# Kernel optimization log

Measured on AMD Instinct MI355X. Metric: run time of the kernel, lower is better.

The kernel has to match this reference:

```python
import jax, jax.numpy as jnp
import numpy as np

D_MODEL = 1024
B, N = 2, 4096
EPS = 1e-4


def setup_inputs() -> dict:
    key = jax.random.key(0)
    ks = jax.random.split(key, 8)
    s = 1.0 / np.sqrt(D_MODEL)
    return {
        "x": jax.random.normal(ks[0], (B, N, D_MODEL), dtype=jnp.float32),
        "Wq": jax.random.normal(ks[1], (D_MODEL, D_MODEL), dtype=jnp.float32) * s,
        "bq": jax.random.normal(ks[2], (D_MODEL,), dtype=jnp.float32) * 0.01,
        "Wk": jax.random.normal(ks[3], (D_MODEL, D_MODEL), dtype=jnp.float32) * s,
        "bk": jax.random.normal(ks[4], (D_MODEL,), dtype=jnp.float32) * 0.01,
        "Wv": jax.random.normal(ks[5], (D_MODEL, D_MODEL), dtype=jnp.float32) * s,
        "bv": jax.random.normal(ks[6], (D_MODEL,), dtype=jnp.float32) * 0.01,
        "alpha": jnp.float32(1.5),
        "lam": jnp.float32(12.0),
    }


def reference(x, Wq, bq, Wk, bk, Wv, bv, alpha, lam):
    # CSOCKernelAttention.forward
    Bb, n, d = x.shape
    # torch nn.Linear: y = x @ W.T + b
    q = jnp.einsum("bnd,ed->bne", x, Wq) + bq
    k = jnp.einsum("bnd,ed->bne", x, Wk) + bk
    v = jnp.einsum("bnd,ed->bne", x, Wv) + bv
    idx = jnp.arange(n, dtype=jnp.float32)
    r = jnp.abs(idx[:, None] - idx[None, :])  # [N, N]
    # K(r) = (r + eps)^(-|alpha|) * exp(-r / |lambda|)
    K = (r + EPS) ** (-jnp.abs(alpha)) * jnp.exp(-r / jnp.abs(lam))  # [N, N]
    logits = jnp.einsum("bqd,bkd->bqk", q, k) / jnp.sqrt(jnp.float32(d))
    logits = logits * K[None]
    attn = jax.nn.softmax(logits, axis=-1)
    out = jnp.einsum("bqk,bkd->bqd", attn, v)
    return (out, attn, K)
```

## Files before the change

### kernel.cpp

```cpp
#include <hip/hip_runtime.h>
#include <hip/hip_bf16.h>
#include <cstdint>
#include <cstddef>

#define D_MODEL 1024
#define SEQ_N   4096
#define BATCH   2
#define BAND    256
#define NELEM   ((size_t)BATCH * SEQ_N * D_MODEL)

typedef __attribute__((ext_vector_type(4))) float  floatx4;
typedef __attribute__((ext_vector_type(8))) short  short8;
typedef __attribute__((ext_vector_type(4))) short  short4v;

__device__ __forceinline__ unsigned short f2bf(float f) {
  unsigned u = __float_as_uint(f);
  u += 0x7FFFu + ((u >> 16) & 1u);
  return (unsigned short)(u >> 16);
}
__device__ __forceinline__ float bf2f(unsigned short u) {
  return __uint_as_float(((unsigned)u) << 16);
}

__global__ __launch_bounds__(256)
void fused_prep(const float* __restrict__ x,
                const float* __restrict__ Wq, const float* __restrict__ Wk,
                const float* __restrict__ Wv, const float* __restrict__ bv,
                const float* __restrict__ alpha_p, const float* __restrict__ lam_p,
                unsigned short* __restrict__ xb,
                unsigned short* __restrict__ Bcat2,
                unsigned short* __restrict__ wqT,
                unsigned short* __restrict__ wkT,
                float* __restrict__ bias2,
                float* __restrict__ K1d)
{
  __shared__ unsigned short Tld[64][66];
  int bid = blockIdx.x, tid = threadIdx.x;
  if (bid < 4096) {
    int i = bid * 256 + tid;
    const floatx4* s4 = (const floatx4*)x;
    floatx4 a = s4[i * 2], b = s4[i * 2 + 1];
    short8 pk;
    pk[0] = (short)f2bf(a[0]); pk[1] = (short)f2bf(a[1]);
    pk[2] = (short)f2bf(a[2]); pk[3] = (short)f2bf(a[3]);
    pk[4] = (short)f2bf(b[0]); pk[5] = (short)f2bf(b[1]);
    pk[6] = (short)f2bf(b[2]); pk[7] = (short)f2bf(b[3]);
    *(short8*)(xb + (size_t)i * 8) = pk;
  } else if (bid < 4608) {
    int i = (bid - 4096) * 256 + tid;
    const floatx4* s4 = (const floatx4*)Wv;
    floatx4 a = s4[i * 2], b = s4[i * 2 + 1];
    short8 pk;
    pk[0] = (short)f2bf(a[0]); pk[1] = (short)f2bf(a[1]);
    pk[2] = (short)f2bf(a[2]); pk[3] = (short)f2bf(a[3]);
    pk[4] = (short)f2bf(b[0]); pk[5] = (short)f2bf(b[1]);
    pk[6] = (short)f2bf(b[2]); pk[7] = (short)f2bf(b[3]);
    *(short8*)(Bcat2 + (size_t)D_MODEL * D_MODEL + (size_t)i * 8) = pk;
  } else if (bid < 5120) {
    int u = bid - 4608;
    const float* src = (u < 256) ? Wq : Wk;
    unsigned short* dst = (u < 256) ? wqT : wkT;
    int t = u & 255;
    int tr = t >> 4, tc = t & 15;
    int rl = tid >> 2, cc = (tid & 3) * 16;
    const float* sp = src + (size_t)(tr * 64 + rl) * D_MODEL + tc * 64 + cc;
#pragma unroll
    for (int q4 = 0; q4 < 4; ++q4) {
      floatx4 v = *(const floatx4*)(sp + q4 * 4);
#pragma unroll
      for (int e = 0; e < 4; ++e) Tld[cc + q4 * 4 + e][rl] = f2bf(v[e]);
    }
    __syncthreads();
    int cl = tid >> 2, rchunk = (tid & 3) * 16;
    short8 o0, o1;
#pragma unroll
    for (int e = 0; e < 8; ++e) { o0[e] = (short)Tld[cl][rchunk + e]; o1[e] = (short)Tld[cl][rchunk + 8 + e]; }
    unsigned short* dp = dst + (size_t)(tc * 64 + cl) * D_MODEL + tr * 64 + rchunk;
    *(short8*)dp = o0;
    *(short8*)(dp + 8) = o1;
  } else {
    int t = (bid - 5120) * 256 + tid;
    if (t < SEQ_N) {
      float a   = fabsf(alpha_p[0]);
      float lam = fabsf(lam_p[0]);
      float rf  = (float)t;
      K1d[t] = powf(rf + 1e-4f, -a) * expf(-rf / lam);
    }
    int v = t - SEQ_N;
    if (v >= 0 && v < D_MODEL) bias2[D_MODEL + v] = bv[v];
  }
}

__global__ __launch_bounds__(256)
void wtilde_kernel(const unsigned short* __restrict__ wkT,
                   const unsigned short* __restrict__ wqT,
                   const float* __restrict__ bq, const float* __restrict__ bk,
                   float* __restrict__ bias2, float* __restrict__ wqv)
{
  const int lane = threadIdx.x & 63, wave = threadIdx.x >> 6;
  const int idx = blockIdx.x * 4 + wave;
  const int d = idx & (D_MODEL - 1);
  const bool isK = idx < D_MODEL;
  const unsigned short* row = (isK ? wkT : wqT) + (size_t)d * D_MODEL + lane * 16;
  const float* b = isK ? bq : bk;
  float s = 0.f;
  short8 v0 = *(const short8*)row, v1 = *(const short8*)(row + 8);
#pragma unroll
  for (int e = 0; e < 8; ++e) {
    s += bf2f((unsigned short)v0[e]) * b[lane * 16 + e];
    s += bf2f((unsigned short)v1[e]) * b[lane * 16 + 8 + e];
  }
#pragma unroll
  for (int o = 32; o; o >>= 1) s += __shfl_xor(s, o);
  if (lane == 0) { if (isK) bias2[d] = s; else wqv[d] = s; }
}

__global__ __launch_bounds__(256)
void rho_kernel(const unsigned short* __restrict__ xb, const float* __restrict__ wqv,
                const float* __restrict__ bq, const float* __restrict__ bk,
                float* __restrict__ rho)
{
  const int lane = threadIdx.x & 63, wave = threadIdx.x >> 6;
  const int gi = blockIdx.x * 4 + wave;
  const unsigned short* xr = xb + (size_t)gi * D_MODEL + lane * 16;
  float s1 = 0.f, s2 = 0.f;
  short8 v0 = *(const short8*)xr, v1 = *(const short8*)(xr + 8);
#pragma unroll
  for (int e = 0; e < 8; ++e) {
    s1 += bf2f((unsigned short)v0[e]) * wqv[lane * 16 + e];
    s1 += bf2f((unsigned short)v1[e]) * wqv[lane * 16 + 8 + e];
  }
#pragma unroll
  for (int e = 0; e < 16; ++e)
    s2 += bq[lane * 16 + e] * bk[lane * 16 + e];
  float s = s1 + s2;
#pragma unroll
  for (int o = 32; o; o >>= 1) s += __shfl_xor(s, o);
  if (lane == 0) rho[gi] = s;
}

__global__ void k1d_kernel(float* __restrict__ K1d,
                           const float* __restrict__ alpha_p,
                           const float* __restrict__ lam_p) {
  int r = blockIdx.x * blockDim.x + threadIdx.x;
  if (r >= SEQ_N) return;
  float a   = fabsf(alpha_p[0]);
  float lam = fabsf(lam_p[0]);
  float rf  = (float)r;
  K1d[r] = powf(rf + 1e-4f, -a) * expf(-rf / lam);
}

__global__ __launch_bounds__(256) void writeK_kernel(float* __restrict__ Kout,
                                                     const float* __restrict__ K1d) {
  size_t t = (size_t)blockIdx.x * 256 + threadIdx.x;
  size_t f = t * 4;
  int i = (int)(f >> 12);
  int j = (int)(f & 4095);
  floatx4 v;
#pragma unroll
  for (int e = 0; e < 4; ++e) {
    int d = i - (j + e); d = d < 0 ? -d : d;
    v[e] = K1d[d];
  }
  __builtin_nontemporal_store(v, (floatx4*)(Kout + f));
}

__global__ __launch_bounds__(256)
void gemm64_mt(const unsigned short* __restrict__ A,
               const unsigned short* __restrict__ B,
               unsigned short* __restrict__ C)
{
  __shared__ unsigned short As[64 * 32];
  __shared__ unsigned short Bs[64 * 32];
  const int tid = threadIdx.x, lane = tid & 63, wave = tid >> 6;
  int gx = (int)gridDim.x;
  int total = gx * (int)gridDim.y;
  int flat  = (int)blockIdx.y * gx + (int)blockIdx.x;
  int w     = (flat & 7) * (total >> 3) + (flat >> 3);
  int bx = w % gx, by = w / gx;
  const int bm0 = by * 64, bn0 = bx * 64;
  const int wm = (wave >> 1) * 32, wn = (wave & 1) * 32;

  floatx4 acc[2][2] = {};
  for (int k0 = 0; k0 < D_MODEL; k0 += 32) {
    {
      int bu = wave * 64;
      int u  = bu + lane;
      const unsigned short* srcA = A + (size_t)(bm0 + (u >> 2)) * D_MODEL + k0 + (u & 3) * 8;
      __builtin_amdgcn_global_load_lds((const __attribute__((address_space(1))) void*)srcA,
                                       (__attribute__((address_space(3))) void*)(As + bu * 8), 16, 0, 0);
      const unsigned short* srcB = B + (size_t)(bn0 + (u >> 2)) * D_MODEL + k0 + (u & 3) * 8;
      __builtin_amdgcn_global_load_lds((const __attribute__((address_space(1))) void*)srcB,
                                       (__attribute__((address_space(3))) void*)(Bs + bu * 8), 16, 0, 0);
    }
    __syncthreads();
    short8 af[2], bf[2];
#pragma unroll
    for (int i = 0; i < 2; ++i)
      af[i] = *(const short8*)(As + (wm + i * 16 + (lane & 15)) * 32 + (lane >> 4) * 8);
#pragma unroll
    for (int j = 0; j < 2; ++j)
      bf[j] = *(const short8*)(Bs + (wn + j * 16 + (lane & 15)) * 32 + (lane >> 4) * 8);
#pragma unroll
    for (int i = 0; i < 2; ++i)
#pragma unroll
      for (int j = 0; j < 2; ++j)
        acc[i][j] = __builtin_amdgcn_mfma_f32_16x16x32_bf16(af[i], bf[j], acc[i][j], 0, 0, 0);
    __syncthreads();
  }
#pragma unroll
  for (int i = 0; i < 2; ++i) {
#pragma unroll
    for (int j = 0; j < 2; ++j) {
      int col   = bn0 + wn + j * 16 + (lane & 15);
      int rbase = bm0 + wm + i * 16 + (lane >> 4) * 4;
#pragma unroll
      for (int r = 0; r < 4; ++r)
        C[(size_t)(rbase + r) * D_MODEL + col] = f2bf(acc[i][j][r]);
    }
  }
}

__global__ __launch_bounds__(256)
void uv_gemm(const unsigned short* __restrict__ xb,
             const unsigned short* __restrict__ Bcat2,
             const float* __restrict__ bias2,
             unsigned short* __restrict__ ub,
             unsigned short* __restrict__ vT)
{
  __shared__ unsigned short As[128 * 64];
  __shared__ unsigned short Bs[128 * 64];
  const int tid = threadIdx.x, lane = tid & 63, wave = tid >> 6;

  int gx = (int)gridDim.x, gy = (int)gridDim.y;
  int total = gx * gy;
  int flat  = (int)blockIdx.y * gx + (int)blockIdx.x;
  int w     = (flat & 7) * (total >> 3) + (flat >> 3);
  int bx = w % gx, by = w / gx;
  const int bm0 = by * 128;
  const int bn0 = bx * 128;
  const int wm = (wave >> 1) * 64, wn = (wave & 1) * 64;
  const bool isU = (bn0 < D_MODEL);

  floatx4 acc[4][4] = {};
  for (int k0 = 0; k0 < D_MODEL; k0 += 64) {
#pragma unroll
    for (int t = 0; t < 4; ++t) {
      int bu  = wave * 64 + t * 256;
      int u   = bu + lane;
      int row = u >> 3;
      int c   = (u & 7) ^ (row & 7);
      const unsigned short* srcA = xb + (size_t)(bm0 + row) * D_MODEL + k0 + c * 8;
      __builtin_amdgcn_global_load_lds((const __attribute__((address_space(1))) void*)srcA,
                                       (__attribute__((address_space(3))) void*)(As + bu * 8), 16, 0, 0);
      const unsigned short* srcB = Bcat2 + (size_t)(bn0 + row) * D_MODEL + k0 + c * 8;
      __builtin_amdgcn_global_load_lds((const __attribute__((address_space(1))) void*)srcB,
                                       (__attribute__((address_space(3))) void*)(Bs + bu * 8), 16, 0, 0);
    }
    __syncthreads();
#pragma unroll
    for (int s = 0; s < 2; ++s) {
      short8 af[4], bf[4];
#pragma unroll
      for (int i = 0; i < 4; ++i) {
        int row = wm + i * 16 + (lane & 15);
        int pc  = (s * 4 + (lane >> 4)) ^ (row & 7);
        af[i] = *(const short8*)(As + row * 64 + pc * 8);
      }
#pragma unroll
      for (int j = 0; j < 4; ++j) {
        int row = wn + j * 16 + (lane & 15);
        int pc  = (s * 4 + (lane >> 4)) ^ (row & 7);
        bf[j] = *(const short8*)(Bs + row * 64 + pc * 8);
      }
      if (isU) {
#pragma unroll
        for (int i = 0; i < 4; ++i)
#pragma unroll
          for (int j = 0; j < 4; ++j)
            acc[i][j] = __builtin_amdgcn_mfma_f32_16x16x32_bf16(bf[j], af[i], acc[i][j], 0, 0, 0);
      } else {
#pragma unroll
        for (int i = 0; i < 4; ++i)
#pragma unroll
          for (int j = 0; j < 4; ++j)
            acc[i][j] = __builtin_amdgcn_mfma_f32_16x16x32_bf16(af[i], bf[j], acc[i][j], 0, 0, 0);
      }
    }
    __syncthreads();
  }

  if (isU) {
#pragma unroll
    for (int i = 0; i < 4; ++i) {
#pragma unroll
      for (int j = 0; j < 4; ++j) {
        int xrow = bm0 + wm + i * 16 + (lane & 15);
        int n0   = bn0 + wn + j * 16 + (lane >> 4) * 4;
        floatx4 b4 = *(const floatx4*)(bias2 + n0);
        short4v pk;
#pragma unroll
        for (int r = 0; r < 4; ++r) pk[r] = (short)f2bf(acc[i][j][r] + b4[r]);
        *(short4v*)(ub + (size_t)xrow * D_MODEL + n0) = pk;
      }
    }
  } else {
#pragma unroll
    for (int i = 0; i < 4; ++i) {
#pragma unroll
      for (int j = 0; j < 4; ++j) {
        int n     = bn0 + wn + j * 16 + (lane & 15);
        int e     = n - D_MODEL;
        int rbase = bm0 + wm + i * 16 + (lane >> 4) * 4;
        float b = bias2[n];
        short4v pk;
#pragma unroll
        for (int r = 0; r < 4; ++r) pk[r] = (short)f2bf(acc[i][j][r] + b);
        *(short4v*)(vT + (size_t)e * (BATCH * SEQ_N) + rbase) = pk;
      }
    }
  }
}

__global__ __launch_bounds__(256)
void band_logits(const unsigned short* __restrict__ U,
                 const unsigned short* __restrict__ Xb,
                 const float* __restrict__ rho,
                 float* __restrict__ Sband,
                 const float* __restrict__ K1d)
{
  __shared__ unsigned short As[64 * 64];
  __shared__ unsigned short Bs[128 * 64];
  const int tid = threadIdx.x, lane = tid & 63, wave = tid >> 6;
  const int bx = blockIdx.x;
  const int g  = blockIdx.y;
  const int z  = blockIdx.z;
  const int bm0 = g * 64;
  const int bn0 = g * 64 - 64 + bx * 128;
  const int wm = (wave >> 1) * 32, wn = (wave & 1) * 64;

  const unsigned short* Ag = U  + (size_t)z * SEQ_N * D_MODEL;
  const unsigned short* Bg = Xb + (size_t)z * SEQ_N * D_MODEL;

  floatx4 acc[2][4] = {};
  for (int k0 = 0; k0 < D_MODEL; k0 += 64) {
#pragma unroll
    for (int t = 0; t < 2; ++t) {
      int bu  = wave * 64 + t * 256;
      int u   = bu + lane;
      int row = u >> 3;
      int c   = (u & 7) ^ (row & 7);
      const unsigned short* srcA = Ag + (size_t)(bm0 + row) * D_MODEL + k0 + c * 8;
      __builtin_amdgcn_global_load_lds((const __attribute__((address_space(1))) void*)srcA,
                                       (__attribute__((address_space(3))) void*)(As + bu * 8), 16, 0, 0);
    }
#pragma unroll
    for (int t = 0; t < 4; ++t) {
      int bu  = wave * 64 + t * 256;
      int u   = bu + lane;
      int row = u >> 3;
      int c   = (u & 7) ^ (row & 7);
      const unsigned short* srcB = Bg + (long)(bn0 + row) * D_MODEL + k0 + c * 8;
      __builtin_amdgcn_global_load_lds((const __attribute__((address_space(1))) void*)srcB,
                                       (__attribute__((address_space(3))) void*)(Bs + bu * 8), 16, 0, 0);
    }
    __syncthreads();
#pragma unroll
    for (int s = 0; s < 2; ++s) {
      short8 af[2], bf[4];
#pragma unroll
      for (int i = 0; i < 2; ++i) {
        int row = wm + i * 16 + (lane & 15);
        int pc  = (s * 4 + (lane >> 4)) ^ (row & 7);
        af[i] = *(const short8*)(As + row * 64 + pc * 8);
      }
#pragma unroll
      for (int j = 0; j < 4; ++j) {
        int row = wn + j * 16 + (lane & 15);
        int pc  = (s * 4 + (lane >> 4)) ^ (row & 7);
        bf[j] = *(const short8*)(Bs + row * 64 + pc * 8);
      }
#pragma unroll
      for (int i = 0; i < 2; ++i)
#pragma unroll
        for (int j = 0; j < 4; ++j)
          acc[i][j] = __builtin_amdgcn_mfma_f32_16x16x32_bf16(af[i], bf[j], acc[i][j], 0, 0, 0);
    }
    __syncthreads();
  }

  float* Cb = Sband + ((size_t)z * SEQ_N + bm0) * BAND + bx * 128;
#pragma unroll
  for (int i = 0; i < 2; ++i) {
    int rl0 = wm + i * 16 + (lane >> 4) * 4;
    float rr[4];
#pragma unroll
    for (int r = 0; r < 4; ++r) rr[r] = rho[(size_t)z * SEQ_N + bm0 + rl0 + r];
#pragma unroll
    for (int j = 0; j < 4; ++j) {
      int cl  = wn + j * 16 + (lane & 15);
#pragma unroll
      for (int r = 0; r < 4; ++r) {
        int col = bn0 + cl;
        int d = (bm0 + rl0 + r) - col; d = d < 0 ? -d : d;
        float v = ((unsigned)col < (unsigned)SEQ_N)
                    ? (acc[i][j][r] + rr[r]) * 0.03125f * K1d[d] : 0.f;
        Cb[(size_t)(rl0 + r) * BAND + cl] = v;
      }
    }
  }
}

__global__ __launch_bounds__(256)
void softmax_band(const float* __restrict__ Sband,
                  float* __restrict__ attn,
                  unsigned short* __restrict__ Pb,
                  float* __restrict__ c_arr)
{
  __shared__ float lds_e[4][BAND];
  const int lane = threadIdx.x & 63, wave = threadIdx.x >> 6;
  const int gi = blockIdx.x * 4 + wave;
  const int ii = gi & (SEQ_N - 1);
  const int g  = ii >> 6;
  const int cbase = g * 64 - 64;
  const float* S = Sband + (size_t)gi * BAND;

  float sv[4];
  float m = 0.0f;
#pragma unroll
  for (int j = 0; j < 4; ++j) {
    int t = j * 64 + lane;
    int col = cbase + t;
    sv[j] = S[t];
    if ((unsigned)col < (unsigned)SEQ_N) m = fmaxf(m, sv[j]);
  }
#pragma unroll
  for (int o = 32; o; o >>= 1) m = fmaxf(m, __shfl_xor(m, o));

  float s = 0.f;
#pragma unroll
  for (int j = 0; j < 4; ++j) {
    int t = j * 64 + lane;
    int col = cbase + t;
    float e = ((unsigned)col < (unsigned)SEQ_N) ? __expf(sv[j] - m) : 0.f;
    sv[j] = e;
    s += e;
  }
#pragma unroll
  for (int o = 32; o; o >>= 1) s += __shfl_xor(s, o);

  int n_valid = BAND - ((g == 0) ? 64 : 0) - ((g == 63) ? 64 : 0);
  float efar  = __expf(-m);
  float denom = s + (float)(SEQ_N - n_valid) * efar;
  float inv   = 1.0f / denom;
  float c     = efar * inv;

  unsigned short* prow = Pb + (size_t)gi * BAND;
#pragma unroll
  for (int j = 0; j < 4; ++j) {
    int t = j * 64 + lane;
    float p = sv[j] * inv;
    lds_e[wave][t] = p;
    int col = cbase + t;
    prow[t] = ((unsigned)col < (unsigned)SEQ_N) ? f2bf(p - c) : (unsigned short)0;
  }
  if (lane == 0) c_arr[gi] = c;

  float* arow = attn + (size_t)gi * SEQ_N;
#pragma unroll
  for (int jj = 0; jj < 16; ++jj) {
    int col0 = jj * 256 + lane * 4;
    floatx4 o;
#pragma unroll
    for (int e = 0; e < 4; ++e) {
      int t = col0 + e - cbase;
      o[e] = ((unsigned)t < (unsigned)BAND) ? lds_e[wave][t] : c;
    }
    __builtin_nontemporal_store(o, (floatx4*)(arow + col0));
  }
}

__global__ __launch_bounds__(256)
void colsumv_kernel(const unsigned short* __restrict__ vT, float* __restrict__ colsumV) {
  const int lane = threadIdx.x & 63, wave = threadIdx.x >> 6;
  const int idx = blockIdx.x * 4 + wave;
  const int d = idx >> 1, b = idx & 1;
  const unsigned short* p = vT + (size_t)d * (BATCH * SEQ_N) + b * SEQ_N;
  float s = 0.f;
#pragma unroll
  for (int it = 0; it < 8; ++it) {
    short8 v = *(const short8*)(p + (size_t)(it * 512 + lane * 8));
#pragma unroll
    for (int e = 0; e < 8; ++e) s += bf2f((unsigned short)v[e]);
  }
#pragma unroll
  for (int o = 32; o; o >>= 1) s += __shfl_xor(s, o);
  if (lane == 0) colsumV[b * D_MODEL + d] = s;
}

__global__ __launch_bounds__(256)
void band_pv(const unsigned short* __restrict__ Pb,
             const unsigned short* __restrict__ vT,
             const float* __restrict__ c_arr,
             const float* __restrict__ colsumV,
             float* __restrict__ outp)
{
  __shared__ unsigned short As[64 * 64];
  __shared__ unsigned short Bs[128 * 64];
  const int tid = threadIdx.x, lane = tid & 63, wave = tid >> 6;
  const int bx = blockIdx.x;
  const int g  = blockIdx.y;
  const int z  = blockIdx.z;
  const int bm0 = g * 64;
  const int bn0 = bx * 128;
  const int wm = (wave >> 1) * 32, wn = (wave & 1) * 64;

  const unsigned short* Ag = Pb + ((size_t)z * SEQ_N + bm0) * BAND;
  const unsigned short* Bg = vT + (long)z * SEQ_N + (long)bm0 - 64;

  floatx4 acc[2][4] = {};
  for (int k0 = 0; k0 < BAND; k0 += 64) {
#pragma unroll
    for (int t = 0; t < 2; ++t) {
      int bu  = wave * 64 + t * 256;
      int u   = bu + lane;
      int row = u >> 3;
      int c   = (u & 7) ^ (row & 7);
      const unsigned short* srcA = Ag + (size_t)row * BAND + k0 + c * 8;
      __builtin_amdgcn_global_load_lds((const __attribute__((address_space(1))) void*)srcA,
                                       (__attribute__((address_space(3))) void*)(As + bu * 8), 16, 0, 0);
    }
#pragma unroll
    for (int t = 0; t < 4; ++t) {
      int bu  = wave * 64 + t * 256;
      int u   = bu + lane;
      int row = u >> 3;
      int c   = (u & 7) ^ (row & 7);
      const unsigned short* srcB = Bg + (size_t)(bn0 + row) * (BATCH * SEQ_N) + k0 + c * 8;
      __builtin_amdgcn_global_load_lds((const __attribute__((address_space(1))) void*)srcB,
                                       (__attribute__((address_space(3))) void*)(Bs + bu * 8), 16, 0, 0);
    }
    __syncthreads();
#pragma unroll
    for (int s = 0; s < 2; ++s) {
      short8 af[2], bf[4];
#pragma unroll
      for (int i = 0; i < 2; ++i) {
        int row = wm + i * 16 + (lane & 15);
        int pc  = (s * 4 + (lane >> 4)) ^ (row & 7);
        af[i] = *(const short8*)(As + row * 64 + pc * 8);
      }
#pragma unroll
      for (int j = 0; j < 4; ++j) {
        int row = wn + j * 16 + (lane & 15);
        int pc  = (s * 4 + (lane >> 4)) ^ (row & 7);
        bf[j] = *(const short8*)(Bs + row * 64 + pc * 8);
      }
#pragma unroll
      for (int i = 0; i < 2; ++i)
#pragma unroll
        for (int j = 0; j < 4; ++j)
          acc[i][j] = __builtin_amdgcn_mfma_f32_16x16x32_bf16(af[i], bf[j], acc[i][j], 0, 0, 0);
    }
    __syncthreads();
  }

#pragma unroll
  for (int i = 0; i < 2; ++i) {
#pragma unroll
    for (int j = 0; j < 4; ++j) {
      int col   = bn0 + wn + j * 16 + (lane & 15);
      int rbase = bm0 + wm + i * 16 + (lane >> 4) * 4;
      float csv = colsumV[z * D_MODEL + col];
#pragma unroll
      for (int r = 0; r < 4; ++r) {
        int row = rbase + r;
        float o = acc[i][j][r] + c_arr[(size_t)z * SEQ_N + row] * csv;
        __builtin_nontemporal_store(o, outp + ((size_t)z * SEQ_N + row) * D_MODEL + col);
      }
    }
  }
}

#define BM 128
#define BN 128
#define BK 32

template<int ASRC, int BSRC, int EPI>
__global__ __launch_bounds__(256)
void gemm_bt(const void* __restrict__ Ap_, int lda, long sA,
             const void* __restrict__ Bp_, int ldb, long sB,
             void* __restrict__ Cp_, int ldc, long sC,
             int K, const float* __restrict__ bias,
             const float* __restrict__ K1d)
{
  __shared__ unsigned short As[BM * BK];
  __shared__ unsigned short Bs[BN * BK];
  const int tid  = threadIdx.x;
  const int lane = tid & 63;
  const int wave = tid >> 6;

  int gx = (int)gridDim.x, gy = (int)gridDim.y;
  int total = gx * gy * (int)gridDim.z;
  int flat  = (int)blockIdx.z * gx * gy + (int)blockIdx.y * gx + (int)blockIdx.x;
  int w     = (flat & 7) * (total >> 3) + (flat >> 3);
  int bx = w % gx;
  int t_ = w / gx;
  int by = t_ % gy;
  int z  = t_ / gy;

  const int bm0  = by * BM;
  const int bn0  = bx * BN;
  const int wm   = (wave >> 1) * 64;
  const int wn   = (wave & 1) * 64;

  floatx4 acc[4][4] = {};

  const unsigned short* Agb = (const unsigned short*)Ap_ + (size_t)z * (size_t)sA;
  const float*          Agf = (const float*)Ap_          + (size_t)z * (size_t)sA;
  const unsigned short* Bgb = (const unsigned short*)Bp_ + (size_t)z * (size_t)sB;
  const float*          Bgf = (const float*)Bp_          + (size_t)z * (size_t)sB;

  for (int k0 = 0; k0 < K; k0 += BK) {
    if constexpr (ASRC == 0) {
#pragma unroll
      for (int t = 0; t < 2; ++t) {
        int bu = wave * 64 + t * 256;
        int u  = bu + lane;
        const unsigned short* src = Agb + (size_t)(bm0 + (u >> 2)) * lda + k0 + (u & 3) * 8;
        __builtin_amdgcn_global_load_lds((const __attribute__((address_space(1))) void*)src,
                                         (__attribute__((address_space(3))) void*)(As + bu * 8),
                                         16, 0, 0);
      }
    } else {
#pragma unroll
      for (int t = 0; t < 2; ++t) {
        int u = tid + t * 256;
        const float* src = Agf + (size_t)(bm0 + (u >> 2)) * lda + k0 + (u & 3) * 8;
        floatx4 x0 = *(const floatx4*)src;
        floatx4 x1 = *(const floatx4*)(src + 4);
        short8 pk;
        pk[0] = (short)f2bf(x0[0]); pk[1] = (short)f2bf(x0[1]);
        pk[2] = (short)f2bf(x0[2]); pk[3] = (short)f2bf(x0[3]);
        pk[4] = (short)f2bf(x1[0]); pk[5] = (short)f2bf(x1[1]);
        pk[6] = (short)f2bf(x1[2]); pk[7] = (short)f2bf(x1[3]);
        *(short8*)(As + u * 8) = pk;
      }
    }
    if constexpr (BSRC == 0) {
#pragma unroll
      for (int t = 0; t < 2; ++t) {
        int bu = wave * 64 + t * 256;
        int u  = bu + lane;
        const unsigned short* src = Bgb + (size_t)(bn0 + (u >> 2)) * ldb + k0 + (u & 3) * 8;
        __builtin_amdgcn_global_load_lds((const __attribute__((address_space(1))) void*)src,
                                         (__attribute__((address_space(3))) void*)(Bs + bu * 8),
                                         16, 0, 0);
      }
    } else {
#pragma unroll
      for (int t = 0; t < 2; ++t) {
        int u = tid + t * 256;
        const float* src = Bgf + (size_t)(bn0 + (u >> 2)) * ldb + k0 + (u & 3) * 8;
        floatx4 x0 = *(const floatx4*)src;
        floatx4 x1 = *(const floatx4*)(src + 4);
        short8 pk;
        pk[0] = (short)f2bf(x0[0]); pk[1] = (short)f2bf(x0[1]);
        pk[2] = (short)f2bf(x0[2]); pk[3] = (short)f2bf(x0[3]);
        pk[4] = (short)f2bf(x1[0]); pk[5] = (short)f2bf(x1[1]);
        pk[6] = (short)f2bf(x1[2]); pk[7] = (short)f2bf(x1[3]);
        *(short8*)(Bs + u * 8) = pk;
      }
    }
    __syncthreads();

    short8 af[4], bf[4];
#pragma unroll
    for (int i = 0; i < 4; ++i)
      af[i] = *(const short8*)(As + (wm + i * 16 + (lane & 15)) * BK + (lane >> 4) * 8);
#pragma unroll
    for (int j = 0; j < 4; ++j)
      bf[j] = *(const short8*)(Bs + (wn + j * 16 + (lane & 15)) * BK + (lane >> 4) * 8);
#pragma unroll
    for (int i = 0; i < 4; ++i)
#pragma unroll
      for (int j = 0; j < 4; ++j)
        acc[i][j] = __builtin_amdgcn_mfma_f32_16x16x32_bf16(af[i], bf[j], acc[i][j], 0, 0, 0);
    __syncthreads();
  }

  const int col0 = bn0 + wn;
  const int row0 = bm0 + wm;
#pragma unroll
  for (int i = 0; i < 4; ++i) {
#pragma unroll
    for (int j = 0; j < 4; ++j) {
      int col   = col0 + j * 16 + (lane & 15);
      int rbase = row0 + i * 16 + (lane >> 4) * 4;
      if constexpr (EPI == 0) {
        unsigned short* C = (unsigned short*)Cp_ + (size_t)z * (size_t)sC;
        float b = bias[col];
#pragma unroll
        for (int r = 0; r < 4; ++r)
          C[(size_t)(rbase + r) * ldc + col] = f2bf(acc[i][j][r] + b);
      } else if constexpr (EPI == 1) {
        unsigned short* C = (unsigned short*)Cp_ + (size_t)z * (size_t)sC;
#pragma unroll
        for (int r = 0; r < 4; ++r)
          C[(size_t)(rbase + r) * ldc + col] = f2bf(acc[i][j][r] + bias[rbase + r]);
      } else if constexpr (EPI == 2) {
        float* C = (float*)Cp_ + (size_t)z * (size_t)sC;
#pragma unroll
        for (int r = 0; r < 4; ++r) {
          int row = rbase + r;
          int d = row - col; d = d < 0 ? -d : d;
          C[(size_t)row * ldc + col] = acc[i][j][r] * 0.03125f * K1d[d];
        }
      } else {
        float* C = (float*)Cp_ + (size_t)z * (size_t)sC;
#pragma unroll
        for (int r = 0; r < 4; ++r)
          C[(size_t)(rbase + r) * ldc + col] = acc[i][j][r];
      }
    }
  }
}

__global__ __launch_bounds__(256)
void softmax_kernel(float* __restrict__ attn) {
  const int tid = threadIdx.x;
  float* p = attn + (size_t)blockIdx.x * SEQ_N;
  floatx4* p4 = (floatx4*)p;
  floatx4 x[4];
  float m = -3.402823466e+38f;
#pragma unroll
  for (int c = 0; c < 4; ++c) {
    x[c] = p4[tid + c * 256];
    m = fmaxf(m, fmaxf(fmaxf(x[c][0], x[c][1]), fmaxf(x[c][2], x[c][3])));
  }
#pragma unroll
  for (int o = 32; o; o >>= 1) m = fmaxf(m, __shfl_xor(m, o));
  __shared__ float redm[4], reds[4];
  if ((tid & 63) == 0) redm[tid >> 6] = m;
  __syncthreads();
  m = fmaxf(fmaxf(redm[0], redm[1]), fmaxf(redm[2], redm[3]));
  float s = 0.f;
#pragma unroll
  for (int c = 0; c < 4; ++c)
#pragma unroll
    for (int e = 0; e < 4; ++e) {
      float t = __expf(x[c][e] - m);
      x[c][e] = t;
      s += t;
    }
#pragma unroll
  for (int o = 32; o; o >>= 1) s += __shfl_xor(s, o);
  if ((tid & 63) == 0) reds[tid >> 6] = s;
  __syncthreads();
  s = reds[0] + reds[1] + reds[2] + reds[3];
  float inv = 1.0f / s;
#pragma unroll
  for (int c = 0; c < 4; ++c) {
    floatx4 y;
#pragma unroll
    for (int e = 0; e < 4; ++e) y[e] = x[c][e] * inv;
    p4[tid + c * 256] = y;
  }
}

extern "C" void kernel_launch(void* const* d_in, const int* in_sizes, int n_in,
                              void* d_out, int out_size, void* d_ws, size_t ws_size,
                              hipStream_t stream) {
  const float* x     = (const float*)d_in[0];
  const float* Wq    = (const float*)d_in[1];
  const float* bq    = (const float*)d_in[2];
  const float* Wk    = (const float*)d_in[3];
  const float* bk    = (const float*)d_in[4];
  const float* Wv    = (const float*)d_in[5];
  const float* bv    = (const float*)d_in[6];
  const float* alpha = (const float*)d_in[7];
  const float* lam   = (const float*)d_in[8];

  float* outp  = (float*)d_out;
  float* attnp = outp + (size_t)BATCH * SEQ_N * D_MODEL;
  float* Kp    = attnp + (size_t)BATCH * SEQ_N * SEQ_N;

  char* ws = (char*)d_ws;
  float* K1d = (float*)ws;
  unsigned short* vT   = (unsigned short*)(ws + 16384);
  unsigned short* xb   = vT + NELEM;
  unsigned short* ub   = xb + NELEM;
  unsigned short* wqT  = ub + NELEM;
  unsigned short* wkT  = wqT + (size_t)D_MODEL * D_MODEL;
  unsigned short* Bcat2 = wkT + (size_t)D_MODEL * D_MODEL;
  float* Sband   = (float*)(Bcat2 + (size_t)2 * D_MODEL * D_MODEL);
  unsigned short* Pb = (unsigned short*)(Sband + (size_t)BATCH * SEQ_N * BAND);
  float* c_arr   = (float*)(Pb + (size_t)BATCH * SEQ_N * BAND);
  float* colsumV = c_arr + (size_t)BATCH * SEQ_N;
  float* bias2   = colsumV + (size_t)BATCH * D_MODEL;
  float* wqv     = bias2 + 2 * D_MODEL;
  float* rho     = wqv + D_MODEL;

  size_t need = (size_t)((char*)(rho + BATCH * SEQ_N) - ws);
  const bool fast = ws_size >= need;

  if (fast) {
    fused_prep<<<5140, 256, 0, stream>>>(x, Wq, Wk, Wv, bv, alpha, lam,
                                         xb, Bcat2, wqT, wkT, bias2, K1d);
    writeK_kernel<<<(SEQ_N * SEQ_N / 4) / 256, 256, 0, stream>>>(Kp, K1d);
    wtilde_kernel<<<512, 256, 0, stream>>>(wkT, wqT, bq, bk, bias2, wqv);
    gemm64_mt<<<dim3(16, 16), 256, 0, stream>>>(wkT, wqT, Bcat2);
    rho_kernel<<<BATCH * SEQ_N / 4, 256, 0, stream>>>(xb, wqv, bq, bk, rho);
    uv_gemm<<<dim3(16, 64), 256, 0, stream>>>(xb, Bcat2, bias2, ub, vT);
    colsumv_kernel<<<BATCH * D_MODEL / 4, 256, 0, stream>>>(vT, colsumV);
    band_logits<<<dim3(2, SEQ_N / 64, BATCH), 256, 0, stream>>>(ub, xb, rho, Sband, K1d);
    softmax_band<<<BATCH * SEQ_N / 4, 256, 0, stream>>>(Sband, attnp, Pb, c_arr);
    band_pv<<<dim3(D_MODEL / 128, SEQ_N / 64, BATCH), 256, 0, stream>>>(
        Pb, vT, c_arr, colsumV, outp);
  } else {
    unsigned short* qb = xb;
    unsigned short* kb = ub;
    k1d_kernel<<<16, 256, 0, stream>>>(K1d, alpha, lam);
    writeK_kernel<<<(SEQ_N * SEQ_N / 4) / 256, 256, 0, stream>>>(Kp, K1d);
    gemm_bt<1, 1, 0><<<dim3(D_MODEL / BN, BATCH * SEQ_N / BM, 1), 256, 0, stream>>>(
        x, D_MODEL, 0, Wq, D_MODEL, 0, qb, D_MODEL, 0, D_MODEL, bq, nullptr);
    gemm_bt<1, 1, 0><<<dim3(D_MODEL / BN, BATCH * SEQ_N / BM, 1), 256, 0, stream>>>(
        x, D_MODEL, 0, Wk, D_MODEL, 0, kb, D_MODEL, 0, D_MODEL, bk, nullptr);
    gemm_bt<1, 1, 1><<<dim3(BATCH * SEQ_N / BN, D_MODEL / BM, 1), 256, 0, stream>>>(
        Wv, D_MODEL, 0, x, D_MODEL, 0, vT, BATCH * SEQ_N, 0, D_MODEL, bv, nullptr);
    gemm_bt<0, 0, 2><<<dim3(SEQ_N / BN, SEQ_N / BM, BATCH), 256, 0, stream>>>(
        qb, D_MODEL, (long)SEQ_N * D_MODEL, kb, D_MODEL, (long)SEQ_N * D_MODEL,
        attnp, SEQ_N, (long)SEQ_N * SEQ_N, D_MODEL, nullptr, K1d);
    softmax_kernel<<<BATCH * SEQ_N, 256, 0, stream>>>(attnp);
    gemm_bt<1, 0, 3><<<dim3(D_MODEL / BN, SEQ_N / BM, BATCH), 256, 0, stream>>>(
        attnp, SEQ_N, (long)SEQ_N * SEQ_N, vT, BATCH * SEQ_N, (long)SEQ_N,
        outp, D_MODEL, (long)SEQ_N * D_MODEL, SEQ_N, nullptr, nullptr);
  }
}
```

Baseline: 168.4 us.

## Double-buffer LDS tiles in uv_gemm and band_logits to overlap loads with MFMA

Converts the single-buffered K-loop in the uv projection GEMM and the band logits GEMM into a two-stage ping-pong pipeline. The next tile's global-to-LDS loads are issued before computing the current tile, and a partial vmcnt wait lets those loads stay in flight during the MFMAs. This targets the load latency that was exposed between barriers. LDS use per block doubles, which may reduce occupancy.

```diff
diff --git a/kernel.cpp b/kernel.cpp
--- a/kernel.cpp
+++ b/kernel.cpp
@@ -228,8 +228,8 @@
              unsigned short* __restrict__ ub,
              unsigned short* __restrict__ vT)
 {
-  __shared__ unsigned short As[128 * 64];
-  __shared__ unsigned short Bs[128 * 64];
+  __shared__ unsigned short As[2][128 * 64];
+  __shared__ unsigned short Bs[2][128 * 64];
   const int tid = threadIdx.x, lane = tid & 63, wave = tid >> 6;
 
   int gx = (int)gridDim.x, gy = (int)gridDim.y;
@@ -243,21 +243,25 @@
   const bool isU = (bn0 < D_MODEL);
 
   floatx4 acc[4][4] = {};
-  for (int k0 = 0; k0 < D_MODEL; k0 += 64) {
+
+  auto stage = [&](int buf, int kt) {
+    int k0s = kt * 64;
 #pragma unroll
     for (int t = 0; t < 4; ++t) {
       int bu  = wave * 64 + t * 256;
       int u   = bu + lane;
       int row = u >> 3;
       int c   = (u & 7) ^ (row & 7);
-      const unsigned short* srcA = xb + (size_t)(bm0 + row) * D_MODEL + k0 + c * 8;
-      __builtin_amdgcn_global_load_lds((const __attribute__((address_space(1))) void*)srcA,
-                                       (__attribute__((address_space(3))) void*)(As + bu * 8), 16, 0, 0);
-      const unsigned short* srcB = Bcat2 + (size_t)(bn0 + row) * D_MODEL + k0 + c * 8;
-      __builtin_amdgcn_global_load_lds((const __attribute__((address_space(1))) void*)srcB,
-                                       (__attribute__((address_space(3))) void*)(Bs + bu * 8), 16, 0, 0);
-    }
-    __syncthreads();
+      const unsigned short* sA = xb + (size_t)(bm0 + row) * D_MODEL + k0s + c * 8;
+      __builtin_amdgcn_global_load_lds((const __attribute__((address_space(1))) void*)sA,
+                                       (__attribute__((address_space(3))) void*)(&As[buf][bu * 8]), 16, 0, 0);
+      const unsigned short* sB = Bcat2 + (size_t)(bn0 + row) * D_MODEL + k0s + c * 8;
+      __builtin_amdgcn_global_load_lds((const __attribute__((address_space(1))) void*)sB,
+                                       (__attribute__((address_space(3))) void*)(&Bs[buf][bu * 8]), 16, 0, 0);
+    }
+  };
+
+  auto compute = [&](int buf) {
 #pragma unroll
     for (int s = 0; s < 2; ++s) {
       short8 af[4], bf[4];
@@ -265,13 +269,13 @@
       for (int i = 0; i < 4; ++i) {
         int row = wm + i * 16 + (lane & 15);
         int pc  = (s * 4 + (lane >> 4)) ^ (row & 7);
-        af[i] = *(const short8*)(As + row * 64 + pc * 8);
+        af[i] = *(const short8*)(&As[buf][row * 64 + pc * 8]);
       }
 #pragma unroll
       for (int j = 0; j < 4; ++j) {
         int row = wn + j * 16 + (lane & 15);
         int pc  = (s * 4 + (lane >> 4)) ^ (row & 7);
-        bf[j] = *(const short8*)(Bs + row * 64 + pc * 8);
+        bf[j] = *(const short8*)(&Bs[buf][row * 64 + pc * 8]);
       }
       if (isU) {
 #pragma unroll
@@ -287,8 +291,22 @@
             acc[i][j] = __builtin_amdgcn_mfma_f32_16x16x32_bf16(af[i], bf[j], acc[i][j], 0, 0, 0);
       }
     }
-    __syncthreads();
-  }
+  };
+
+  stage(0, 0);
+#pragma unroll 1
+  for (int kt = 0; kt < 15; ++kt) {
+    stage((kt + 1) & 1, kt + 1);
+    asm volatile("s_waitcnt vmcnt(8)" ::: "memory");
+    __builtin_amdgcn_sched_barrier(0);
+    __builtin_amdgcn_s_barrier();
+    compute(kt & 1);
+    __builtin_amdgcn_s_barrier();
+  }
+  asm volatile("s_waitcnt vmcnt(0)" ::: "memory");
+  __builtin_amdgcn_sched_barrier(0);
+  __builtin_amdgcn_s_barrier();
+  compute(1);
 
   if (isU) {
 #pragma unroll
@@ -329,8 +347,8 @@
                  float* __restrict__ Sband,
                  const float* __restrict__ K1d)
 {
-  __shared__ unsigned short As[64 * 64];
-  __shared__ unsigned short Bs[128 * 64];
+  __shared__ unsigned short As[2][64 * 64];
+  __shared__ unsigned short Bs[2][128 * 64];
   const int tid = threadIdx.x, lane = tid & 63, wave = tid >> 6;
   const int bx = blockIdx.x;
   const int g  = blockIdx.y;
@@ -343,16 +361,18 @@
   const unsigned short* Bg = Xb + (size_t)z * SEQ_N * D_MODEL;
 
   floatx4 acc[2][4] = {};
-  for (int k0 = 0; k0 < D_MODEL; k0 += 64) {
+
+  auto stage = [&](int buf, int kt) {
+    int k0s = kt * 64;
 #pragma unroll
     for (int t = 0; t < 2; ++t) {
       int bu  = wave * 64 + t * 256;
       int u   = bu + lane;
       int row = u >> 3;
       int c   = (u & 7) ^ (row & 7);
-      const unsigned short* srcA = Ag + (size_t)(bm0 + row) * D_MODEL + k0 + c * 8;
-      __builtin_amdgcn_global_load_lds((const __attribute__((address_space(1))) void*)srcA,
-                                       (__attribute__((address_space(3))) void*)(As + bu * 8), 16, 0, 0);
+      const unsigned short* sA = Ag + (size_t)(bm0 + row) * D_MODEL + k0s + c * 8;
+      __builtin_amdgcn_global_load_lds((const __attribute__((address_space(1))) void*)sA,
+                                       (__attribute__((address_space(3))) void*)(&As[buf][bu * 8]), 16, 0, 0);
     }
 #pragma unroll
     for (int t = 0; t < 4; ++t) {
@@ -360,11 +380,13 @@
       int u   = bu + lane;
       int row = u >> 3;
       int c   = (u & 7) ^ (row & 7);
-      const unsigned short* srcB = Bg + (long)(bn0 + row) * D_MODEL + k0 + c * 8;
-      __builtin_amdgcn_global_load_lds((const __attribute__((address_space(1))) void*)srcB,
-                                       (__attribute__((address_space(3))) void*)(Bs + bu * 8), 16, 0, 0);
-    }
-    __syncthreads();
+      const unsigned short* sB = Bg + (long)(bn0 + row) * D_MODEL + k0s + c * 8;
+      __builtin_amdgcn_global_load_lds((const __attribute__((address_space(1))) void*)sB,
+                                       (__attribute__((address_space(3))) void*)(&Bs[buf][bu * 8]), 16, 0, 0);
+    }
+  };
+
+  auto compute = [&](int buf) {
 #pragma unroll
     for (int s = 0; s < 2; ++s) {
       short8 af[2], bf[4];
@@ -372,13 +394,13 @@
       for (int i = 0; i < 2; ++i) {
         int row = wm + i * 16 + (lane & 15);
         int pc  = (s * 4 + (lane >> 4)) ^ (row & 7);
-        af[i] = *(const short8*)(As + row * 64 + pc * 8);
+        af[i] = *(const short8*)(&As[buf][row * 64 + pc * 8]);
       }
 #pragma unroll
       for (int j = 0; j < 4; ++j) {
         int row = wn + j * 16 + (lane & 15);
         int pc  = (s * 4 + (lane >> 4)) ^ (row & 7);
-        bf[j] = *(const short8*)(Bs + row * 64 + pc * 8);
+        bf[j] = *(const short8*)(&Bs[buf][row * 64 + pc * 8]);
       }
 #pragma unroll
       for (int i = 0; i < 2; ++i)
@@ -386,8 +408,22 @@
         for (int j = 0; j < 4; ++j)
           acc[i][j] = __builtin_amdgcn_mfma_f32_16x16x32_bf16(af[i], bf[j], acc[i][j], 0, 0, 0);
     }
-    __syncthreads();
-  }
+  };
+
+  stage(0, 0);
+#pragma unroll 1
+  for (int kt = 0; kt < 15; ++kt) {
+    stage((kt + 1) & 1, kt + 1);
+    asm volatile("s_waitcnt vmcnt(6)" ::: "memory");
+    __builtin_amdgcn_sched_barrier(0);
+    __builtin_amdgcn_s_barrier();
+    compute(kt & 1);
+    __builtin_amdgcn_s_barrier();
+  }
+  asm volatile("s_waitcnt vmcnt(0)" ::: "memory");
+  __builtin_amdgcn_sched_barrier(0);
+  __builtin_amdgcn_s_barrier();
+  compute(1);
 
   float* Cb = Sband + ((size_t)z * SEQ_N + bm0) * BAND + bx * 128;
 #pragma unroll
```

Result: no change. 169.0 us (+0.4%).
